# Kernel optimization log

Hardware: AMD Instinct MI355X
Metric: run time of the kernel (lower is better)

Reference implementation:

```python
import jax, jax.numpy as jnp
import numpy as np

B, N, DIM, H, DH = 4, 2048, 512, 8, 64
INNER = H * DH  # 512
SCALE = DH ** -0.5


def setup_inputs() -> dict:
    key = jax.random.key(0)
    k1, k2, k3, k4 = jax.random.split(key, 4)
    x = jax.random.normal(k1, (B, N, DIM), dtype=jnp.float32)
    bias = jax.random.normal(k2, (B, N, DIM), dtype=jnp.float32)
    # to_qkv: Linear(dim, inner*3, bias=False)
    w_qkv = jax.random.normal(k3, (DIM, 3 * INNER), dtype=jnp.float32) * (DIM ** -0.5)
    # to_out: Linear(inner, dim) with bias (project_out=True since heads != 1)
    w_out = jax.random.normal(k4, (INNER, DIM), dtype=jnp.float32) * (INNER ** -0.5)
    b_out = jnp.zeros((DIM,), dtype=jnp.float32)
    return {"x": x, "bias": bias, "w_qkv": w_qkv, "w_out": w_out, "b_out": b_out}


def _split_heads(t):
    # [b, n, h*d] -> [b, h, n, d]
    b, n, _ = t.shape
    return t.reshape(b, n, H, DH).transpose(0, 2, 1, 3)


def reference(x, bias, w_qkv, w_out, b_out):
    qkv = x @ w_qkv  # [b, n, 3*inner]
    q, k, v = jnp.split(qkv, 3, axis=-1)
    q, k, v = map(_split_heads, (q, k, v))
    dots = jnp.einsum('bhid,bhjd->bhij', q, k) * SCALE  # [b,h,n,n]

    qkv_b = bias @ w_qkv
    qb, kb, _ = jnp.split(qkv_b, 3, axis=-1)
    qb, kb = _split_heads(qb), _split_heads(kb)
    dots = dots + jnp.einsum('bhid,bhjd->bhij', qb, kb) * SCALE

    attn = jax.nn.softmax(dots, axis=-1)
    out = jnp.einsum('bhij,bhjd->bhid', attn, v)  # [b,h,n,d]
    out = out.transpose(0, 2, 1, 3).reshape(x.shape[0], x.shape[1], INNER)
    return out @ w_out + b_out
```

## Files before the change

kernel.cpp:

```cpp
#include <hip/hip_runtime.h>
#include <hip/hip_bf16.h>

#define DEV __device__ __forceinline__

typedef __attribute__((ext_vector_type(8))) short short8;
typedef __attribute__((ext_vector_type(4))) int i32x4;
typedef __attribute__((ext_vector_type(2))) int i32x2;
typedef __attribute__((ext_vector_type(4))) float f32x4;
typedef __attribute__((ext_vector_type(16))) float f32x16;

constexpr int B = 4, N = 2048, H = 8, DH = 64;
constexpr int INNER = H * DH;
constexpr int BH = B * H;
constexpr float SCALE = 0.125f;

constexpr size_t OFF_WQKVT = 0;
constexpr size_t OFF_WOUTT = OFF_WQKVT + (size_t)1536 * 512;
constexpr size_t OFF_QT    = OFF_WOUTT + (size_t)512 * 512;
constexpr size_t OFF_KT    = OFF_QT + (size_t)BH * N * 128;
constexpr size_t OFF_VT    = OFF_KT + (size_t)BH * N * 128;
constexpr size_t OFF_AO    = OFF_VT + (size_t)BH * DH * N;
constexpr size_t OFF_XBF   = OFF_AO + (size_t)8192 * 512;
constexpr size_t OFF_BBF   = OFF_AO;

DEV short f2b(float f) {
    __hip_bfloat16 h = __float2bfloat16(f);
    return __builtin_bit_cast(short, h);
}

DEV int cvtpk(float lo, float hi) {
    int r;
    asm("v_cvt_pk_bf16_f32 %0, %1, %2" : "=v"(r) : "v"(lo), "v"(hi));
    return r;
}

DEV void plswap(int& a, int& b) {
    i32x2 r = __builtin_amdgcn_permlane32_swap(a, b, false, false);
    a = r.x; b = r.y;
}

DEV void gload16(const void* g, void* l) {
    __builtin_amdgcn_global_load_lds(
        (const __attribute__((address_space(1))) unsigned int*)g,
        (__attribute__((address_space(3))) unsigned int*)l, 16, 0, 0);
}

__global__ void prep_kernel(const float* __restrict__ wqkv,
                            const float* __restrict__ wout,
                            const float* __restrict__ x,
                            const float* __restrict__ bias,
                            __hip_bfloat16* __restrict__ ws) {
    __hip_bfloat16* wqkvT = ws + OFF_WQKVT;
    __hip_bfloat16* woutT = ws + OFF_WOUTT;
    short8* xbf = (short8*)(ws + OFF_XBF);
    short8* bbf = (short8*)(ws + OFF_BBF);
    int tid = blockIdx.x * blockDim.x + threadIdx.x;
    const int nconv = 8192 * 512 / 8;
    const int t1 = 512 * 1536 / 4;
    const int t2 = 512 * 512 / 4;
    const int total = 2 * nconv + t1 + t2;
    for (int i = tid; i < total; i += gridDim.x * blockDim.x) {
        if (i < 2 * nconv) {
            const float4* src = (const float4*)(i < nconv ? x : bias);
            short8* dst = i < nconv ? xbf : bbf;
            int j = i < nconv ? i : i - nconv;
            float4 v0 = src[2 * j], v1 = src[2 * j + 1];
            short8 sv;
            sv[0] = f2b(v0.x); sv[1] = f2b(v0.y); sv[2] = f2b(v0.z); sv[3] = f2b(v0.w);
            sv[4] = f2b(v1.x); sv[5] = f2b(v1.y); sv[6] = f2b(v1.z); sv[7] = f2b(v1.w);
            dst[j] = sv;
        } else if (i < 2 * nconv + t1) {
            int j = i - 2 * nconv;
            int k  = j / 384;
            int c4 = (j % 384) * 4;
            float4 v = ((const float4*)wqkv)[j];
            wqkvT[(size_t)(c4 + 0) * 512 + k] = __float2bfloat16(v.x);
            wqkvT[(size_t)(c4 + 1) * 512 + k] = __float2bfloat16(v.y);
            wqkvT[(size_t)(c4 + 2) * 512 + k] = __float2bfloat16(v.z);
            wqkvT[(size_t)(c4 + 3) * 512 + k] = __float2bfloat16(v.w);
        } else {
            int j = i - 2 * nconv - t1;
            int k  = j / 128;
            int c4 = (j % 128) * 4;
            float4 v = ((const float4*)wout)[j];
            woutT[(size_t)(c4 + 0) * 512 + k] = __float2bfloat16(v.x);
            woutT[(size_t)(c4 + 1) * 512 + k] = __float2bfloat16(v.y);
            woutT[(size_t)(c4 + 2) * 512 + k] = __float2bfloat16(v.z);
            woutT[(size_t)(c4 + 3) * 512 + k] = __float2bfloat16(v.w);
        }
    }
}

__global__ __launch_bounds__(256) void gemm_qkv(__hip_bfloat16* __restrict__ ws) {
    int mt = blockIdx.x, yt = blockIdx.y;
    bool src_is_bias = (yt >= 12);
    int nt = src_is_bias ? yt - 12 : yt;
    const short* A  = (const short*)(ws + (src_is_bias ? OFF_BBF : OFF_XBF));
    const short* Bt = (const short*)(ws + OFF_WQKVT);
    int m0 = mt * 128, n0 = nt * 128;

    __shared__ __align__(16) short As[128][64];
    __shared__ __align__(16) short Bs[128][64];

    int tid  = threadIdx.x;
    int wave = tid >> 6, lane = tid & 63;
    int wrow = wave >> 1, wcol = wave & 1;
    int lg = lane >> 4, li = lane & 15;

    f32x4 acc[4][4] = {};

    for (int k0 = 0; k0 < 512; k0 += 64) {
#pragma unroll
        for (int i = 0; i < 4; ++i) {
            int c = wave * 4 + i;
            int r = c * 8 + (lane >> 3);
            gload16((const char*)A + ((size_t)(m0 + r) * 512 + k0 + (lane & 7) * 8) * 2,
                    (char*)&As[0][0] + c * 1024);
            gload16((const char*)Bt + ((size_t)(n0 + r) * 512 + k0 + (lane & 7) * 8) * 2,
                    (char*)&Bs[0][0] + c * 1024);
        }
        __syncthreads();
#pragma unroll
        for (int ks = 0; ks < 2; ++ks) {
            short8 af[4], bf[4];
#pragma unroll
            for (int m = 0; m < 4; ++m)
                af[m] = *(const short8*)(&As[wrow * 64 + m * 16 + li][ks * 32 + lg * 8]);
#pragma unroll
            for (int n = 0; n < 4; ++n)
                bf[n] = *(const short8*)(&Bs[wcol * 64 + n * 16 + li][ks * 32 + lg * 8]);
#pragma unroll
            for (int m = 0; m < 4; ++m)
#pragma unroll
                for (int n = 0; n < 4; ++n)
                    acc[m][n] = __builtin_amdgcn_mfma_f32_16x16x32_bf16(af[m], bf[n], acc[m][n], 0, 0, 0);
        }
        __syncthreads();
    }

    __hip_bfloat16* QT = ws + OFF_QT;
    __hip_bfloat16* KT = ws + OFF_KT;
    __hip_bfloat16* VT = ws + OFF_VT;
    int qkoff = src_is_bias ? 64 : 0;
#pragma unroll
    for (int m = 0; m < 4; ++m)
#pragma unroll
        for (int n = 0; n < 4; ++n)
#pragma unroll
            for (int j = 0; j < 4; ++j) {
                int row = m0 + wrow * 64 + m * 16 + lg * 4 + j;
                int col = n0 + wcol * 64 + n * 16 + li;
                float v = acc[m][n][j];
                int b = row >> 11, nn = row & 2047;
                if (col < 512) {
                    int h = col >> 6, d = col & 63;
                    QT[((size_t)(b * H + h) * N + nn) * 128 + d + qkoff] = __float2bfloat16(v * SCALE);
                } else if (col < 1024) {
                    int c = col - 512; int h = c >> 6, d = c & 63;
                    KT[((size_t)(b * H + h) * N + nn) * 128 + d + qkoff] = __float2bfloat16(v);
                } else {
                    int c = col - 1024; int h = c >> 6, d = c & 63;
                    VT[((size_t)(b * H + h) * DH + d) * N + nn] = __float2bfloat16(v);
                }
            }
}

__global__ __launch_bounds__(256, 3) void attn_kernel(__hip_bfloat16* __restrict__ ws) {
    int bid = blockIdx.x;
    int c   = bid & 7;
    int idx = bid >> 3;
    int bh  = (idx & 3) * 8 + c;
    int qb  = idx >> 2;

    int wave = threadIdx.x >> 6, lane = threadIdx.x & 63;
    int li32 = lane & 31, hi = lane >> 5;
    int qr0 = qb * 128 + wave * 32;

    const short* QT  = (const short*)(ws + OFF_QT) + (size_t)bh * N * 128;
    const char*  KTg = (const char*)((const short*)(ws + OFF_KT) + (size_t)bh * N * 128);
    const char*  VTg = (const char*)((const short*)(ws + OFF_VT) + (size_t)bh * DH * N);

    __shared__ __align__(16) short Ktile[2][64][128];
    __shared__ __align__(16) short Vtile[2][64][64];

    short8 qf[8];
#pragma unroll
    for (int kc = 0; kc < 8; ++kc)
        qf[kc] = *(const short8*)(QT + (size_t)(qr0 + li32) * 128 + kc * 16 + hi * 8);

    float m_run = -3e38f, l_run = 0.f;
    f32x16 o[2] = {};

    auto stage = [&](int t, int b) {
        int kv0 = t * 64;
#pragma unroll
        for (int cc = 0; cc < 4; ++cc) {
            int ck = wave * 4 + cc;
            int r  = ck * 4 + (lane >> 4);
            int cbx = (lane & 15) * 16;
            gload16(KTg + (size_t)(kv0 + r) * 256 + (cbx ^ ((r & 7) << 4)),
                    (char*)&Ktile[b][0][0] + ck * 1024);
        }
#pragma unroll
        for (int cc = 0; cc < 2; ++cc) {
            int ck = wave * 2 + cc;
            int r  = ck * 8 + (lane >> 3);
            int cbx = (lane & 7) * 16;
            gload16(VTg + (size_t)r * 4096 + kv0 * 2 + (cbx ^ ((r & 7) << 4)),
                    (char*)&Vtile[b][0][0] + ck * 1024);
        }
    };

    stage(0, 0);
    __syncthreads();
    int buf = 0;

    for (int t = 0; t < N / 64; ++t) {
        if (t + 1 < N / 64) stage(t + 1, buf ^ 1);
        const char* Kb = (const char*)&Ktile[buf][0][0];
        const char* Vb = (const char*)&Vtile[buf][0][0];

        f32x16 sT[2] = {};
        __builtin_amdgcn_s_setprio(1);
#pragma unroll
        for (int sub = 0; sub < 2; ++sub) {
            int row = sub * 32 + li32;
            int sw  = (row & 7) << 4;
            const char* kbase = Kb + row * 256;
#pragma unroll
            for (int kc = 0; kc < 8; ++kc) {
                short8 kf = *(const short8*)(kbase + ((kc * 32 + hi * 16) ^ sw));
                sT[sub] = __builtin_amdgcn_mfma_f32_32x32x16_bf16(kf, qf[kc], sT[sub], 0, 0, 0);
            }
        }
        __builtin_amdgcn_s_setprio(0);

        float pm = sT[0][0];
#pragma unroll
        for (int sub = 0; sub < 2; ++sub)
#pragma unroll
            for (int r = 0; r < 16; ++r) pm = fmaxf(pm, sT[sub][r]);
        pm = fmaxf(pm, __shfl_xor(pm, 32));

        if (__any(pm > m_run + 8.f)) {
            float mn = fmaxf(m_run, pm);
            float al = __expf(m_run - mn);
#pragma unroll
            for (int a = 0; a < 2; ++a)
#pragma unroll
                for (int r = 0; r < 16; ++r) o[a][r] *= al;
            l_run *= al;
            m_run = mn;
        }

        float ls = 0.f;
        int w[2][8];
#pragma unroll
        for (int sub = 0; sub < 2; ++sub)
#pragma unroll
            for (int r2 = 0; r2 < 8; ++r2) {
                float p0 = __expf(sT[sub][2 * r2]     - m_run);
                float p1 = __expf(sT[sub][2 * r2 + 1] - m_run);
                ls += p0 + p1;
                w[sub][r2] = cvtpk(p0, p1);
            }
        ls += __shfl_xor(ls, 32);
        l_run += ls;

        short8 pf[2][2];
#pragma unroll
        for (int sub = 0; sub < 2; ++sub) {
            plswap(w[sub][0], w[sub][2]); plswap(w[sub][1], w[sub][3]);
            plswap(w[sub][4], w[sub][6]); plswap(w[sub][5], w[sub][7]);
            i32x4 f0 = { w[sub][0], w[sub][1], w[sub][2], w[sub][3] };
            i32x4 f1 = { w[sub][4], w[sub][5], w[sub][6], w[sub][7] };
            pf[sub][0] = __builtin_bit_cast(short8, f0);
            pf[sub][1] = __builtin_bit_cast(short8, f1);
        }

        __builtin_amdgcn_s_setprio(1);
#pragma unroll
        for (int sub = 0; sub < 2; ++sub)
#pragma unroll
            for (int ksel = 0; ksel < 2; ++ksel) {
                int cc = sub * 2 + ksel;
#pragma unroll
                for (int a = 0; a < 2; ++a) {
                    int row = a * 32 + li32;
                    int sw  = (row & 7) << 4;
                    short8 vf = *(const short8*)(Vb + row * 128 + ((cc * 32 + hi * 16) ^ sw));
                    o[a] = __builtin_amdgcn_mfma_f32_32x32x16_bf16(vf, pf[sub][ksel], o[a], 0, 0, 0);
                }
            }
        __builtin_amdgcn_s_setprio(0);

        __syncthreads();
        buf ^= 1;
    }

    __hip_bfloat16* AO = ws + OFF_AO;
    int b = bh >> 3, h = bh & 7;
    char* tb = (char*)&Ktile[0][0][0] + wave * 4096;
    float inv = 1.f / l_run;
#pragma unroll
    for (int a = 0; a < 2; ++a)
#pragma unroll
        for (int r2 = 0; r2 < 8; ++r2) {
            int r = 2 * r2;
            int dv = (r & 3) + 8 * (r >> 2) + 4 * hi + 32 * a;
            int word = cvtpk(o[a][r] * inv, o[a][r + 1] * inv);
            *(int*)(tb + li32 * 128 + ((dv * 2) ^ ((li32 & 7) << 4))) = word;
        }
#pragma unroll
    for (int qq = 0; qq < 32; qq += 8) {
        int q = qq + (lane >> 3), seg = lane & 7;
        short8 vrow = *(const short8*)(tb + q * 128 + ((seg * 16) ^ ((q & 7) << 4)));
        *(short8*)(AO + (size_t)(b * N + qr0 + q) * INNER + h * 64 + seg * 8) = vrow;
    }
}

__global__ __launch_bounds__(256) void gemm_out(const __hip_bfloat16* __restrict__ ws_c,
                                                const float* __restrict__ bout,
                                                float* __restrict__ out) {
    const short* AO = (const short*)(ws_c + OFF_AO);
    const short* Bt = (const short*)(ws_c + OFF_WOUTT);
    int m0 = blockIdx.x * 128, n0 = blockIdx.y * 128;

    __shared__ __align__(16) short As[128][64];
    __shared__ __align__(16) short Bs[128][64];

    int tid  = threadIdx.x;
    int wave = tid >> 6, lane = tid & 63;
    int wrow = wave >> 1, wcol = wave & 1;
    int lg = lane >> 4, li = lane & 15;

    f32x4 acc[4][4] = {};

    for (int k0 = 0; k0 < 512; k0 += 64) {
#pragma unroll
        for (int i = 0; i < 4; ++i) {
            int c = wave * 4 + i;
            int r = c * 8 + (lane >> 3);
            gload16((const char*)AO + ((size_t)(m0 + r) * 512 + k0 + (lane & 7) * 8) * 2,
                    (char*)&As[0][0] + c * 1024);
            gload16((const char*)Bt + ((size_t)(n0 + r) * 512 + k0 + (lane & 7) * 8) * 2,
                    (char*)&Bs[0][0] + c * 1024);
        }
        __syncthreads();
#pragma unroll
        for (int ks = 0; ks < 2; ++ks) {
            short8 af[4], bf[4];
#pragma unroll
            for (int m = 0; m < 4; ++m)
                af[m] = *(const short8*)(&As[wrow * 64 + m * 16 + li][ks * 32 + lg * 8]);
#pragma unroll
            for (int n = 0; n < 4; ++n)
                bf[n] = *(const short8*)(&Bs[wcol * 64 + n * 16 + li][ks * 32 + lg * 8]);
#pragma unroll
            for (int m = 0; m < 4; ++m)
#pragma unroll
                for (int n = 0; n < 4; ++n)
                    acc[m][n] = __builtin_amdgcn_mfma_f32_16x16x32_bf16(af[m], bf[n], acc[m][n], 0, 0, 0);
        }
        __syncthreads();
    }
#pragma unroll
    for (int m = 0; m < 4; ++m)
#pragma unroll
        for (int n = 0; n < 4; ++n)
#pragma unroll
            for (int j = 0; j < 4; ++j) {
                int row = m0 + wrow * 64 + m * 16 + lg * 4 + j;
                int col = n0 + wcol * 64 + n * 16 + li;
                out[(size_t)row * 512 + col] = acc[m][n][j] + bout[col];
            }
}

extern "C" void kernel_launch(void* const* d_in, const int* in_sizes, int n_in,
                              void* d_out, int out_size, void* d_ws, size_t ws_size,
                              hipStream_t stream) {
    const float* x    = (const float*)d_in[0];
    const float* bias = (const float*)d_in[1];
    const float* wqkv = (const float*)d_in[2];
    const float* wout = (const float*)d_in[3];
    const float* bout = (const float*)d_in[4];
    float* out = (float*)d_out;
    __hip_bfloat16* ws = (__hip_bfloat16*)d_ws;

    hipLaunchKernelGGL(prep_kernel, dim3(2048), dim3(256), 0, stream, wqkv, wout, x, bias, ws);
    hipLaunchKernelGGL(gemm_qkv, dim3(64, 20), dim3(256), 0, stream, ws);
    hipLaunchKernelGGL(attn_kernel, dim3(512), dim3(256), 0, stream, ws);
    hipLaunchKernelGGL(gemm_out, dim3(64, 4), dim3(256), 0, stream, (const __hip_bfloat16*)ws, bout, out);
}
```

Baseline: 145.0 us.

## Software-pipeline QK^T one tile ahead of softmax and use exp2 with folded log2e

Restructures the attention loop so the QK^T MFMAs for tile t+1 are issued before the softmax and PV of tile t, with K and V staged separately at different prefetch distances. The log2(e) factor is folded into the Q scale so the raw v_exp_f32 instruction can replace __expf. The row-max and row-sum reductions become trees instead of serial chains, and launch bounds drop from 3 to 2 blocks per CU. The aim is to overlap the exponential math with matrix work and shorten dependency chains. The cost is extra registers for the second score buffer and lower occupancy.

Result: no change. 144.9 us (-0.0%).

```diff
diff --git a/kernel.cpp b/kernel.cpp
--- a/kernel.cpp
+++ b/kernel.cpp
@@ -12,7 +12,7 @@
 constexpr int B = 4, N = 2048, H = 8, DH = 64;
 constexpr int INNER = H * DH;
 constexpr int BH = B * H;
-constexpr float SCALE = 0.125f;
+constexpr float QSCALE = 0.125f * 1.44269504088896f;
 
 constexpr size_t OFF_WQKVT = 0;
 constexpr size_t OFF_WOUTT = OFF_WQKVT + (size_t)1536 * 512;
@@ -31,6 +31,12 @@
 DEV int cvtpk(float lo, float hi) {
     int r;
     asm("v_cvt_pk_bf16_f32 %0, %1, %2" : "=v"(r) : "v"(lo), "v"(hi));
+    return r;
+}
+
+DEV float fexp2(float x) {
+    float r;
+    asm("v_exp_f32 %0, %1" : "=v"(r) : "v"(x));
     return r;
 }
 
@@ -154,7 +160,7 @@
                 int b = row >> 11, nn = row & 2047;
                 if (col < 512) {
                     int h = col >> 6, d = col & 63;
-                    QT[((size_t)(b * H + h) * N + nn) * 128 + d + qkoff] = __float2bfloat16(v * SCALE);
+                    QT[((size_t)(b * H + h) * N + nn) * 128 + d + qkoff] = __float2bfloat16(v * QSCALE);
                 } else if (col < 1024) {
                     int c = col - 512; int h = c >> 6, d = c & 63;
                     KT[((size_t)(b * H + h) * N + nn) * 128 + d + qkoff] = __float2bfloat16(v);
@@ -165,7 +171,7 @@
             }
 }
 
-__global__ __launch_bounds__(256, 3) void attn_kernel(__hip_bfloat16* __restrict__ ws) {
+__global__ __launch_bounds__(256, 2) void attn_kernel(__hip_bfloat16* __restrict__ ws) {
     int bid = blockIdx.x;
     int c   = bid & 7;
     int idx = bid >> 3;
@@ -191,7 +197,7 @@
     float m_run = -3e38f, l_run = 0.f;
     f32x16 o[2] = {};
 
-    auto stage = [&](int t, int b) {
+    auto stageK = [&](int t, int b) {
         int kv0 = t * 64;
 #pragma unroll
         for (int cc = 0; cc < 4; ++cc) {
@@ -201,6 +207,9 @@
             gload16(KTg + (size_t)(kv0 + r) * 256 + (cbx ^ ((r & 7) << 4)),
                     (char*)&Ktile[b][0][0] + ck * 1024);
         }
+    };
+    auto stageV = [&](int t, int b) {
+        int kv0 = t * 64;
 #pragma unroll
         for (int cc = 0; cc < 2; ++cc) {
             int ck = wave * 2 + cc;
@@ -211,16 +220,12 @@
         }
     };
 
-    stage(0, 0);
-    __syncthreads();
-    int buf = 0;
-
-    for (int t = 0; t < N / 64; ++t) {
-        if (t + 1 < N / 64) stage(t + 1, buf ^ 1);
-        const char* Kb = (const char*)&Ktile[buf][0][0];
-        const char* Vb = (const char*)&Vtile[buf][0][0];
-
-        f32x16 sT[2] = {};
+    auto qkt = [&](f32x16 (&sT)[2], int b) {
+        const char* Kb = (const char*)&Ktile[b][0][0];
+#pragma unroll
+        for (int s2 = 0; s2 < 2; ++s2)
+#pragma unroll
+            for (int r = 0; r < 16; ++r) sT[s2][r] = 0.f;
         __builtin_amdgcn_s_setprio(1);
 #pragma unroll
         for (int sub = 0; sub < 2; ++sub) {
@@ -234,17 +239,24 @@
             }
         }
         __builtin_amdgcn_s_setprio(0);
-
-        float pm = sT[0][0];
-#pragma unroll
-        for (int sub = 0; sub < 2; ++sub)
-#pragma unroll
-            for (int r = 0; r < 16; ++r) pm = fmaxf(pm, sT[sub][r]);
+    };
+
+    auto step = [&](f32x16 (&cur)[2], f32x16 (&next)[2], int t, bool doK, bool doNext) {
+        if (doK)    stageK(t + 2, t & 1);
+        if (doNext) stageV(t + 1, (t + 1) & 1);
+        if (doNext) qkt(next, (t + 1) & 1);
+
+        float t0[8];
+#pragma unroll
+        for (int j = 0; j < 8; ++j)
+            t0[j] = fmaxf(fmaxf(cur[0][j], cur[0][j + 8]), fmaxf(cur[1][j], cur[1][j + 8]));
+        float pm = fmaxf(fmaxf(fmaxf(t0[0], t0[1]), fmaxf(t0[2], t0[3])),
+                         fmaxf(fmaxf(t0[4], t0[5]), fmaxf(t0[6], t0[7])));
         pm = fmaxf(pm, __shfl_xor(pm, 32));
 
         if (__any(pm > m_run + 8.f)) {
             float mn = fmaxf(m_run, pm);
-            float al = __expf(m_run - mn);
+            float al = fexp2(m_run - mn);
 #pragma unroll
             for (int a = 0; a < 2; ++a)
 #pragma unroll
@@ -253,17 +265,18 @@
             m_run = mn;
         }
 
-        float ls = 0.f;
+        float lsp[4] = {0.f, 0.f, 0.f, 0.f};
         int w[2][8];
 #pragma unroll
         for (int sub = 0; sub < 2; ++sub)
 #pragma unroll
             for (int r2 = 0; r2 < 8; ++r2) {
-                float p0 = __expf(sT[sub][2 * r2]     - m_run);
-                float p1 = __expf(sT[sub][2 * r2 + 1] - m_run);
-                ls += p0 + p1;
+                float p0 = fexp2(cur[sub][2 * r2]     - m_run);
+                float p1 = fexp2(cur[sub][2 * r2 + 1] - m_run);
+                lsp[r2 & 3] += p0 + p1;
                 w[sub][r2] = cvtpk(p0, p1);
             }
+        float ls = (lsp[0] + lsp[1]) + (lsp[2] + lsp[3]);
         ls += __shfl_xor(ls, 32);
         l_run += ls;
 
@@ -278,6 +291,7 @@
             pf[sub][1] = __builtin_bit_cast(short8, f1);
         }
 
+        const char* Vb = (const char*)&Vtile[t & 1][0][0];
         __builtin_amdgcn_s_setprio(1);
 #pragma unroll
         for (int sub = 0; sub < 2; ++sub)
@@ -295,8 +309,22 @@
         __builtin_amdgcn_s_setprio(0);
 
         __syncthreads();
-        buf ^= 1;
+    };
+
+    stageK(0, 0);
+    stageV(0, 0);
+    stageK(1, 1);
+    __syncthreads();
+    f32x16 sA[2], sB[2];
+    qkt(sA, 0);
+    __syncthreads();
+
+    for (int t = 0; t < 30; t += 2) {
+        step(sA, sB, t,     true, true);
+        step(sB, sA, t + 1, true, true);
     }
+    step(sA, sB, 30, false, true);
+    step(sB, sA, 31, false, false);
 
     __hip_bfloat16* AO = ws + OFF_AO;
     int b = bh >> 3, h = bh & 7;
```
